# Kernel tuning notes

Measured on AMD Instinct MI355X. Metric: run time of the kernel, lower is better.

Reference implementation:

```python
import jax, jax.numpy as jnp
import numpy as np

# norse LIFParameters defaults
ALPHA = 100.0        # superspike surrogate slope
DT = 1e-3
TAU_SYN_INV = 200.0  # 1/5e-3
TAU_MEM_INV = 100.0  # 1/1e-2
V_TH = 1.0           # v_leak = v_reset = 0

@jax.custom_vjp
def heaviside(v):
    # forward: hard threshold; backward: superspike surrogate 1/(alpha*|v|+1)^2
    return (v > 0).astype(v.dtype)

def _hv_fwd(v):
    return heaviside(v), v

def _hv_bwd(v, g):
    return (g / (ALPHA * jnp.abs(v) + 1.0) ** 2,)

heaviside.defvjp(_hv_fwd, _hv_bwd)

def setup_inputs() -> dict:
    key = jax.random.key(0)
    ks = jax.random.split(key, 5)
    B, H, W, O = 2048, 15, 15, 10
    x = jax.random.uniform(ks[0], (B, 1, H, W), jnp.float32)  # image-like in [0,1)
    conv_w = jax.random.normal(ks[1], (2, 1, 4, 4), jnp.float32) * 0.25
    conv_b = jax.random.normal(ks[2], (2,), jnp.float32) * 0.1
    lin_w = jax.random.normal(ks[3], (O, 72), jnp.float32) * (1.0 / np.sqrt(72.0))
    lin_b = jax.random.normal(ks[4], (O,), jnp.float32) * 0.1
    return {"x": x, "conv_w": conv_w, "conv_b": conv_b,
            "lin_w": lin_w, "lin_b": lin_b, "num_steps": 300}

def reference(x, conv_w, conv_b, lin_w, lin_b, num_steps):
    B = x.shape[0]
    O = lin_w.shape[0]
    current = x * 10.0  # constant input current to the encoder

    def step(carry, _):
        v_enc, v, i = carry
        # --- constant_current_lif_encode step (lif_current_encoder) ---
        v_enc = v_enc + DT * TAU_MEM_INV * (-v_enc + current)
        z_in = heaviside(v_enc - V_TH)
        v_enc = v_enc - z_in * v_enc  # reset to v_reset = 0
        # --- feed-forward: conv -> maxpool(2) -> linear ---
        c = jax.lax.conv_general_dilated(
            z_in, conv_w, (1, 1), 'VALID',
            dimension_numbers=('NCHW', 'OIHW', 'NCHW')) + conv_b[None, :, None, None]
        p = jax.lax.reduce_window(c, -jnp.inf, jax.lax.max,
                                  (1, 1, 2, 2), (1, 1, 2, 2), 'VALID')  # [B,2,6,6]
        lin = p.reshape(B, -1) @ lin_w.T + lin_b  # [B,O]
        # --- norse LIFCell (lif_feed_forward_step) ---
        v_dec = v + DT * TAU_MEM_INV * (-v + i)
        i_dec = i - DT * TAU_SYN_INV * i
        spk = heaviside(v_dec - V_TH)
        v_new = (1.0 - spk) * v_dec  # v_reset = 0
        i_new = i_dec + lin
        return (v_enc, v_new, i_new), (spk, v_new)

    init = (jnp.zeros_like(current),
            jnp.zeros((B, O), x.dtype),
            jnp.zeros((B, O), x.dtype))
    _, (spk_rec, mem_rec) = jax.lax.scan(step, init, None, length=num_steps)
    spk_out = spk_rec.sum(0)  # [B,O]
    return spk_out, mem_rec, spk_rec
```

## Files before the change

kernel.cpp:

```cpp
#include <hip/hip_runtime.h>
#include <math.h>


typedef float v2f __attribute__((ext_vector_type(2)));

__global__ __launch_bounds__(128, 4) void snn_step_kernel(
    const float* __restrict__ x,
    const float* __restrict__ conv_w,
    const float* __restrict__ conv_b,
    const float* __restrict__ lin_w,
    const float* __restrict__ lin_b,
    float* __restrict__ out,
    int T, int B)
{
    const int b   = blockIdx.x;
    const int tid = threadIdx.x;
    const int w   = tid & 63;
    const int wv  = tid >> 6;

    __shared__ float    s_linw[720];
    __shared__ float    s_linb[10];
    __shared__ float4   s_lut[4][32];
    __shared__ unsigned s_bits[16][8];
    __shared__ float    s_p[16][80];

    for (int j = tid; j < 720; j += 128) s_linw[j] = lin_w[j];
    if (tid < 10) s_linb[tid] = lin_b[tid];
    {
        const int ky = tid >> 5, n = tid & 31;
        float s00 = 0.f, s01 = 0.f, s10 = 0.f, s11 = 0.f;
#pragma unroll
        for (int kx = 0; kx < 4; ++kx) {
            const float w0 = conv_w[ky * 4 + kx];
            const float w1 = conv_w[16 + ky * 4 + kx];
            if ((n >> kx) & 1)       { s00 += w0; s01 += w1; }
            if ((n >> (kx + 1)) & 1) { s10 += w0; s11 += w1; }
        }
        s_lut[ky][n] = make_float4(s00, s01, s10, s11);
    }
    __syncthreads();

    v2f ve01 = (v2f){0.f, 0.f}, ve23 = (v2f){0.f, 0.f};
    v2f cur01, cur23;
    {
        const int jrow = w >> 4, col = w & 15;
        float c[4];
#pragma unroll
        for (int k = 0; k < 4; ++k) {
            const int  row = 4 * k + jrow;
            const bool act = (col < 15) && (row < 15) && (wv == 0);
            c[k] = act ? __fmul_rn(x[(size_t)b * 225 + row * 15 + col], 10.0f) : 0.f;
        }
        cur01 = (v2f){c[0], c[1]};
        cur23 = (v2f){c[2], c[3]};
    }

    const bool convlane = (w < 36);
    const int  py = w / 6, px = w - 6 * py;
    const int  wordsel = py;
    const int  shx = 2 * px, shx16 = shx + 16;
    const int  off0 = (w < 18) ? w : (w + 2);
    const v2f  cb2 = (v2f){conv_b[0], conv_b[1]};

    const int lo = w >> 2, lq = w & 3;
    v2f lw2[9];
#pragma unroll
    for (int jj = 0; jj < 9; ++jj) {
        int i0 = lo * 72 + lq * 18 + 2 * jj;
        int i1 = i0 + 1;
        lw2[jj] = (v2f){s_linw[i0 < 720 ? i0 : 719],
                        s_linw[i1 < 720 ? i1 : 719]};
    }
    const float lbias = s_linb[lo < 10 ? lo : 0];
    float v = 0.f, i_syn = 0.f, sc = 0.f;
    float svv[6], svs[6];
    const size_t BO = (size_t)B * 10;
    float* mp  = out + BO + (size_t)b * 10 + lo;
    float* spp = out + BO + (size_t)T * BO + (size_t)b * 10 + lo;

    auto enc_pack = [&](int slot) {
        const v2f tenth = (v2f){0.1f, 0.1f};
        v2f vn01 = ve01 + (cur01 - ve01) * tenth;
        v2f vn23 = ve23 + (cur23 - ve23) * tenth;
        bool sp0 = (vn01.x > 1.0f);
        bool sp1 = (vn01.y > 1.0f);
        bool sp2 = (vn23.x > 1.0f);
        bool sp3 = (vn23.y > 1.0f);
        unsigned long long bal0 = __ballot(sp0);
        unsigned long long bal1 = __ballot(sp1);
        unsigned long long bal2 = __ballot(sp2);
        unsigned long long bal3 = __ballot(sp3);
        ve01 = (v2f){sp0 ? 0.f : vn01.x, sp1 ? 0.f : vn01.y};
        ve23 = (v2f){sp2 ? 0.f : vn23.x, sp3 ? 0.f : vn23.y};
        unsigned long long m01 = (w & 2) ? bal1 : bal0;
        unsigned long long m23 = (w & 2) ? bal3 : bal2;
        unsigned long long m   = (w & 4) ? m23 : m01;
        unsigned word = (unsigned)((w & 1) ? (m >> 32) : m);
        if (w < 8) s_bits[slot][w] = word;
    };

    auto conv_compute = [&](int slot, unsigned wb0, unsigned wb1, unsigned wb2) {
        const int i0 = (wb0 >> shx)   & 31;
        const int i1 = (wb0 >> shx16) & 31;
        const int i2 = (wb1 >> shx)   & 31;
        const int i3 = (wb1 >> shx16) & 31;
        const int i4 = (wb2 >> shx)   & 31;

        const float4 f0 = s_lut[0][i0];
        const float4 f1 = s_lut[1][i1];
        const float4 f2 = s_lut[2][i2];
        const float4 f3 = s_lut[3][i3];
        const float4 g0 = s_lut[0][i1];
        const float4 g1 = s_lut[1][i2];
        const float4 g2 = s_lut[2][i3];
        const float4 g3 = s_lut[3][i4];

        v2f a00 = (v2f){f0.x, f0.y};  a00 += (v2f){f1.x, f1.y};
        a00 += (v2f){f2.x, f2.y};     a00 += (v2f){f3.x, f3.y};
        v2f a01 = (v2f){f0.z, f0.w};  a01 += (v2f){f1.z, f1.w};
        a01 += (v2f){f2.z, f2.w};     a01 += (v2f){f3.z, f3.w};
        v2f a10 = (v2f){g0.x, g0.y};  a10 += (v2f){g1.x, g1.y};
        a10 += (v2f){g2.x, g2.y};     a10 += (v2f){g3.x, g3.y};
        v2f a11 = (v2f){g0.z, g0.w};  a11 += (v2f){g1.z, g1.w};
        a11 += (v2f){g2.z, g2.w};     a11 += (v2f){g3.z, g3.w};

        v2f mraw = __builtin_elementwise_max(
                       __builtin_elementwise_max(a00, a01),
                       __builtin_elementwise_max(a10, a11));
        v2f m2 = mraw + cb2;

        float* pbuf = s_p[slot];
        pbuf[off0]      = m2.x;
        pbuf[off0 + 40] = m2.y;
    };

    auto lin_dec = [&](int s, int k) {
        const v2f* pp = (const v2f*)&s_p[s & 15][lq * 20];
        v2f pv[9];
#pragma unroll
        for (int jj = 0; jj < 9; ++jj) pv[jj] = pp[jj];
        v2f pacc = (v2f){0.f, 0.f};
#pragma unroll
        for (int jj = 0; jj < 9; ++jj)
            pacc = __builtin_elementwise_fma(lw2[jj], pv[jj], pacc);
        float partial = __fadd_rn(pacc.x, pacc.y);

        float p1 = __shfl_xor(partial, 1);
        float p2 = __shfl_xor(partial, 2);
        float p3 = __shfl_xor(partial, 3);
        float lin = __fadd_rn(
            __fadd_rn(__fadd_rn(__fadd_rn(partial, p1), p2), p3), lbias);

        float vd  = __fadd_rn(v, __fmul_rn(0.1f, __fsub_rn(i_syn, v)));
        float id  = __fsub_rn(i_syn, __fmul_rn(0.2f, i_syn));
        float spk = (vd > 1.0f) ? 1.0f : 0.0f;
        v = (vd > 1.0f) ? 0.0f : vd;
        sc += spk;
        svv[k] = v;
        svs[k] = spk;
        i_syn = __fadd_rn(id, lin);
    };

    auto issue_stores = [&]() {
        if (lq == 0 && lo < 10) {
#pragma unroll
            for (int k = 0; k < 6; ++k) {
                mp[(size_t)k * BO]  = svv[k];
                spp[(size_t)k * BO] = svs[k];
            }
        }
        mp  += 6 * BO;
        spp += 6 * BO;
    };

    if (wv == 0) enc_pack(0);

    const int NG = T / 6;

    for (int g = 0; g < NG; ++g) {
        const int base = 6 * g;
        if (wv == 0) {
#pragma unroll
            for (int k = 0; k < 4; ++k) {
                const int s = base + k;
                unsigned wb0 = 0, wb1 = 0, wb2 = 0;
                if (convlane) {
                    const unsigned* bb = &s_bits[s & 15][wordsel];
                    wb0 = bb[0]; wb1 = bb[1]; wb2 = bb[2];
                }
                enc_pack((s + 1) & 15);
                if (convlane) conv_compute(s & 15, wb0, wb1, wb2);
            }
            enc_pack((base + 5) & 15);
            enc_pack((base + 6) & 15);
        } else {
            if (g >= 2) issue_stores();
            if (g >= 1) {
                const int pb = base - 6;
                if (convlane) {
                    const unsigned* ba = &s_bits[(pb + 4) & 15][wordsel];
                    unsigned a0 = ba[0], a1 = ba[1], a2 = ba[2];
                    const unsigned* bc = &s_bits[(pb + 5) & 15][wordsel];
                    unsigned c0 = bc[0], c1 = bc[1], c2 = bc[2];
                    conv_compute((pb + 4) & 15, a0, a1, a2);
                    conv_compute((pb + 5) & 15, c0, c1, c2);
                }
#pragma unroll
                for (int k = 0; k < 6; ++k)
                    lin_dec(pb + k, k);
            }
        }
        __syncthreads();
    }

    if (wv == 1) {
        issue_stores();
        const int pb = 6 * (NG - 1);
        if (convlane) {
            const unsigned* ba = &s_bits[(pb + 4) & 15][wordsel];
            unsigned a0 = ba[0], a1 = ba[1], a2 = ba[2];
            const unsigned* bc = &s_bits[(pb + 5) & 15][wordsel];
            unsigned c0 = bc[0], c1 = bc[1], c2 = bc[2];
            conv_compute((pb + 4) & 15, a0, a1, a2);
            conv_compute((pb + 5) & 15, c0, c1, c2);
        }
#pragma unroll
        for (int k = 0; k < 6; ++k)
            lin_dec(pb + k, k);
        issue_stores();
        if (lq == 0 && lo < 10) out[(size_t)b * 10 + lo] = sc;
    }
}

extern "C" void kernel_launch(void* const* d_in, const int* in_sizes, int n_in,
                              void* d_out, int out_size, void* d_ws, size_t ws_size,
                              hipStream_t stream) {
    const float* x      = (const float*)d_in[0];
    const float* conv_w = (const float*)d_in[1];
    const float* conv_b = (const float*)d_in[2];
    const float* lin_w  = (const float*)d_in[3];
    const float* lin_b  = (const float*)d_in[4];
    float* out = (float*)d_out;

    const int B = in_sizes[0] / 225;
    const int T = (out_size / (B * 10) - 1) / 2;

    snn_step_kernel<<<B, 128, 0, stream>>>(x, conv_w, conv_b, lin_w, lin_b, out, T, B);
}
```

Measured before the change: 199.5 us.

## Pre-expand spike bit windows and interleave pooled features for vector LDS access

The encoder now writes spike bitmask words into an expanded shared layout. Each row slot holds a 4-word window, so conv lanes fetch their three words with a single uint4 LDS load instead of three scalar loads. The pooled conv output layout changes so each lane writes both channels with one 8-byte store. The linear weights are permuted to match, letting lin_dec read its 18 floats with four float4 loads plus one float2. This cuts LDS instruction count on the serial per-timestep path, at the cost of 4x larger bit buffers and more complex index arithmetic.

After: 201.9 us. Within noise of the previous version (+1.2%).

```diff
diff --git a/kernel.cpp b/kernel.cpp
--- a/kernel.cpp
+++ b/kernel.cpp
@@ -21,7 +21,7 @@
     __shared__ float    s_linw[720];
     __shared__ float    s_linb[10];
     __shared__ float4   s_lut[4][32];
-    __shared__ unsigned s_bits[16][8];
+    __shared__ uint4    s_bits4[16][8];
     __shared__ float    s_p[16][80];
 
     for (int j = tid; j < 720; j += 128) s_linw[j] = lin_w[j];
@@ -55,21 +55,24 @@
         cur23 = (v2f){c[2], c[3]};
     }
 
+    const int  jword   = (w >> 2) + (w & 3);
+    const bool wr_bits = (w < 24);
+
     const bool convlane = (w < 36);
     const int  py = w / 6, px = w - 6 * py;
     const int  wordsel = py;
     const int  shx = 2 * px, shx16 = shx + 16;
-    const int  off0 = (w < 18) ? w : (w + 2);
+    const int  poff = 20 * (w / 9) + 2 * (w - 9 * (w / 9));
     const v2f  cb2 = (v2f){conv_b[0], conv_b[1]};
 
     const int lo = w >> 2, lq = w & 3;
     v2f lw2[9];
 #pragma unroll
-    for (int jj = 0; jj < 9; ++jj) {
-        int i0 = lo * 72 + lq * 18 + 2 * jj;
-        int i1 = i0 + 1;
-        lw2[jj] = (v2f){s_linw[i0 < 720 ? i0 : 719],
-                        s_linw[i1 < 720 ? i1 : 719]};
+    for (int t = 0; t < 9; ++t) {
+        int i0 = lo * 72 + 9 * lq + t;
+        int i1 = i0 + 36;
+        lw2[t] = (v2f){s_linw[i0 < 720 ? i0 : 719],
+                       s_linw[i1 < 720 ? i1 : 719]};
     }
     const float lbias = s_linb[lo < 10 ? lo : 0];
     float v = 0.f, i_syn = 0.f, sc = 0.f;
@@ -92,11 +95,13 @@
         unsigned long long bal3 = __ballot(sp3);
         ve01 = (v2f){sp0 ? 0.f : vn01.x, sp1 ? 0.f : vn01.y};
         ve23 = (v2f){sp2 ? 0.f : vn23.x, sp3 ? 0.f : vn23.y};
-        unsigned long long m01 = (w & 2) ? bal1 : bal0;
-        unsigned long long m23 = (w & 2) ? bal3 : bal2;
-        unsigned long long m   = (w & 4) ? m23 : m01;
-        unsigned word = (unsigned)((w & 1) ? (m >> 32) : m);
-        if (w < 8) s_bits[slot][w] = word;
+        const int jh = jword >> 1;
+        unsigned long long m01 = (jh & 1) ? bal1 : bal0;
+        unsigned long long m23 = (jh & 1) ? bal3 : bal2;
+        unsigned long long m   = (jh & 2) ? m23 : m01;
+        unsigned word = (unsigned)((jword & 1) ? (m >> 32) : m);
+        word = (jword < 8) ? word : 0u;
+        if (wr_bits) ((unsigned*)&s_bits4[slot][0])[w] = word;
     };
 
     auto conv_compute = [&](int slot, unsigned wb0, unsigned wb1, unsigned wb2) {
@@ -129,20 +134,26 @@
                        __builtin_elementwise_max(a10, a11));
         v2f m2 = mraw + cb2;
 
-        float* pbuf = s_p[slot];
-        pbuf[off0]      = m2.x;
-        pbuf[off0 + 40] = m2.y;
+        *(v2f*)&s_p[slot][poff] = m2;
     };
 
     auto lin_dec = [&](int s, int k) {
-        const v2f* pp = (const v2f*)&s_p[s & 15][lq * 20];
-        v2f pv[9];
-#pragma unroll
-        for (int jj = 0; jj < 9; ++jj) pv[jj] = pp[jj];
+        const float* base = &s_p[s & 15][lq * 20];
+        float4 q0 = *(const float4*)(base + 0);
+        float4 q1 = *(const float4*)(base + 4);
+        float4 q2 = *(const float4*)(base + 8);
+        float4 q3 = *(const float4*)(base + 12);
+        v2f    q4 = *(const v2f*)(base + 16);
         v2f pacc = (v2f){0.f, 0.f};
-#pragma unroll
-        for (int jj = 0; jj < 9; ++jj)
-            pacc = __builtin_elementwise_fma(lw2[jj], pv[jj], pacc);
+        pacc = __builtin_elementwise_fma(lw2[0], (v2f){q0.x, q0.y}, pacc);
+        pacc = __builtin_elementwise_fma(lw2[1], (v2f){q0.z, q0.w}, pacc);
+        pacc = __builtin_elementwise_fma(lw2[2], (v2f){q1.x, q1.y}, pacc);
+        pacc = __builtin_elementwise_fma(lw2[3], (v2f){q1.z, q1.w}, pacc);
+        pacc = __builtin_elementwise_fma(lw2[4], (v2f){q2.x, q2.y}, pacc);
+        pacc = __builtin_elementwise_fma(lw2[5], (v2f){q2.z, q2.w}, pacc);
+        pacc = __builtin_elementwise_fma(lw2[6], (v2f){q3.x, q3.y}, pacc);
+        pacc = __builtin_elementwise_fma(lw2[7], (v2f){q3.z, q3.w}, pacc);
+        pacc = __builtin_elementwise_fma(lw2[8], q4, pacc);
         float partial = __fadd_rn(pacc.x, pacc.y);
 
         float p1 = __shfl_xor(partial, 1);
@@ -183,13 +194,10 @@
 #pragma unroll
             for (int k = 0; k < 4; ++k) {
                 const int s = base + k;
-                unsigned wb0 = 0, wb1 = 0, wb2 = 0;
-                if (convlane) {
-                    const unsigned* bb = &s_bits[s & 15][wordsel];
-                    wb0 = bb[0]; wb1 = bb[1]; wb2 = bb[2];
-                }
+                uint4 bb = make_uint4(0, 0, 0, 0);
+                if (convlane) bb = s_bits4[s & 15][wordsel];
                 enc_pack((s + 1) & 15);
-                if (convlane) conv_compute(s & 15, wb0, wb1, wb2);
+                if (convlane) conv_compute(s & 15, bb.x, bb.y, bb.z);
             }
             enc_pack((base + 5) & 15);
             enc_pack((base + 6) & 15);
@@ -198,12 +206,10 @@
             if (g >= 1) {
                 const int pb = base - 6;
                 if (convlane) {
-                    const unsigned* ba = &s_bits[(pb + 4) & 15][wordsel];
-                    unsigned a0 = ba[0], a1 = ba[1], a2 = ba[2];
-                    const unsigned* bc = &s_bits[(pb + 5) & 15][wordsel];
-                    unsigned c0 = bc[0], c1 = bc[1], c2 = bc[2];
-                    conv_compute((pb + 4) & 15, a0, a1, a2);
-                    conv_compute((pb + 5) & 15, c0, c1, c2);
+                    uint4 ba = s_bits4[(pb + 4) & 15][wordsel];
+                    uint4 bc = s_bits4[(pb + 5) & 15][wordsel];
+                    conv_compute((pb + 4) & 15, ba.x, ba.y, ba.z);
+                    conv_compute((pb + 5) & 15, bc.x, bc.y, bc.z);
                 }
 #pragma unroll
                 for (int k = 0; k < 6; ++k)
@@ -217,12 +223,10 @@
         issue_stores();
         const int pb = 6 * (NG - 1);
         if (convlane) {
-            const unsigned* ba = &s_bits[(pb + 4) & 15][wordsel];
-            unsigned a0 = ba[0], a1 = ba[1], a2 = ba[2];
-            const unsigned* bc = &s_bits[(pb + 5) & 15][wordsel];
-            unsigned c0 = bc[0], c1 = bc[1], c2 = bc[2];
-            conv_compute((pb + 4) & 15, a0, a1, a2);
-            conv_compute((pb + 5) & 15, c0, c1, c2);
+            uint4 ba = s_bits4[(pb + 4) & 15][wordsel];
+            uint4 bc = s_bits4[(pb + 5) & 15][wordsel];
+            conv_compute((pb + 4) & 15, ba.x, ba.y, ba.z);
+            conv_compute((pb + 5) & 15, bc.x, bc.y, bc.z);
         }
 #pragma unroll
         for (int k = 0; k < 6; ++k)
```
